# Performance work log

Measured on AMD Instinct MI355X. Metric: run time of the kernel, lower is better.

The kernel has to match this reference:

```python
import jax, jax.numpy as jnp
import numpy as np

D_MODEL = 1024
NUM_HEADS = 16
HEAD_DIM = D_MODEL // NUM_HEADS
N = 4096


def setup_inputs() -> dict:
    key = jax.random.key(0)
    k_x, k_wqkv, k_bqkv, k_wo, k_bo = jax.random.split(key, 5)
    s_in = 1.0 / np.sqrt(D_MODEL)
    return {
        "x": jax.random.normal(k_x, (N, D_MODEL), dtype=jnp.float32),
        "w_qkv": jax.random.uniform(k_wqkv, (D_MODEL, 3 * D_MODEL), jnp.float32, -s_in, s_in),
        "b_qkv": jax.random.uniform(k_bqkv, (3 * D_MODEL,), jnp.float32, -s_in, s_in),
        "w_out": jax.random.uniform(k_wo, (D_MODEL, D_MODEL), jnp.float32, -s_in, s_in),
        "b_out": jax.random.uniform(k_bo, (D_MODEL,), jnp.float32, -s_in, s_in),
    }


def reference(x, w_qkv, b_qkv, w_out, b_out) -> jnp.ndarray:
    n, d = x.shape
    scale = HEAD_DIM ** -0.5
    # fused QKV projection: [N, 3D] -> [3, H, N, hd]
    qkv = (x @ w_qkv + b_qkv).reshape(n, 3, NUM_HEADS, HEAD_DIM).transpose(1, 2, 0, 3)
    q, k, v = qkv[0], qkv[1], qkv[2]
    attn = jax.nn.softmax(jnp.einsum("hnd,hmd->hnm", q, k) * scale, axis=-1)
    out = jnp.einsum("hnm,hmd->hnd", attn, v)  # [H, N, hd]
    out = out.transpose(1, 0, 2).reshape(n, d)
    return out @ w_out + b_out
```

## Files before the change

kernel.cpp:

```cpp
#include <hip/hip_runtime.h>
#include <hip/hip_bf16.h>

using bf16_t = __bf16;
using bf16x4 = __attribute__((ext_vector_type(4))) __bf16;
using bf16x8 = __attribute__((ext_vector_type(8))) __bf16;
using f32x4  = __attribute__((ext_vector_type(4))) float;
using f32x16 = __attribute__((ext_vector_type(16))) float;
using u32x2  = __attribute__((ext_vector_type(2))) unsigned;

#define N_TOK 4096
#define DM    1024
#define NH    16
#define HD    64
#define D3    3072

#if __has_builtin(__builtin_amdgcn_exp2f)
#define EXP2(x) __builtin_amdgcn_exp2f(x)
#else
extern "C" float __ocml_native_exp2_f32(float);
#define EXP2(x) __ocml_native_exp2_f32(x)
#endif

__device__ __forceinline__ void gl_lds16(const void* g, void* l) {
  __builtin_amdgcn_global_load_lds((const __attribute__((address_space(1))) void*)g,
                                   (__attribute__((address_space(3))) void*)l, 16, 0, 0);
}

__device__ __forceinline__ unsigned pkbf(float a, float b) {
  unsigned short la = __builtin_bit_cast(unsigned short, (bf16_t)a);
  unsigned short lb = __builtin_bit_cast(unsigned short, (bf16_t)b);
  return (unsigned)la | ((unsigned)lb << 16);
}

__device__ __forceinline__ bf16x8 mk8(unsigned a, unsigned b, unsigned c, unsigned d) {
  union { unsigned u[4]; bf16x8 v; } t;
  t.u[0] = a; t.u[1] = b; t.u[2] = c; t.u[3] = d;
  return t.v;
}

__device__ __forceinline__ void softmax_blk(const f32x16& sv, bf16x8& apA, bf16x8& apB) {
  float pp[16];
  #pragma unroll
  for (int r = 0; r < 16; r++) pp[r] = EXP2(sv[r]);
  unsigned w00 = pkbf(pp[0], pp[1]),   w01 = pkbf(pp[2], pp[3]);
  unsigned w10 = pkbf(pp[4], pp[5]),   w11 = pkbf(pp[6], pp[7]);
  unsigned w20 = pkbf(pp[8], pp[9]),   w21 = pkbf(pp[10], pp[11]);
  unsigned w30 = pkbf(pp[12], pp[13]), w31 = pkbf(pp[14], pp[15]);
  u32x2 r00 = __builtin_amdgcn_permlane32_swap(w00, w10, false, false);
  u32x2 r01 = __builtin_amdgcn_permlane32_swap(w01, w11, false, false);
  u32x2 r10 = __builtin_amdgcn_permlane32_swap(w20, w30, false, false);
  u32x2 r11 = __builtin_amdgcn_permlane32_swap(w21, w31, false, false);
  apA = mk8(r00[0], r01[0], r00[1], r01[1]);
  apB = mk8(r10[0], r11[0], r10[1], r11[1]);
}

__global__ void k_cvt_x(const float* __restrict__ x, bf16_t* __restrict__ xb) {
  int i = (blockIdx.x * blockDim.x + threadIdx.x) * 8;
  float4 f0 = *(const float4*)(x + i);
  float4 f1 = *(const float4*)(x + i + 4);
  bf16x8 v;
  v[0] = (bf16_t)f0.x; v[1] = (bf16_t)f0.y; v[2] = (bf16_t)f0.z; v[3] = (bf16_t)f0.w;
  v[4] = (bf16_t)f1.x; v[5] = (bf16_t)f1.y; v[6] = (bf16_t)f1.z; v[7] = (bf16_t)f1.w;
  *(bf16x8*)(xb + i) = v;
}

__global__ void k_transpose_cvt(const float* __restrict__ in, bf16_t* __restrict__ outh,
                                int R, int C) {
  __shared__ float tile[64][65];
  int r0 = blockIdx.y * 64, c0 = blockIdx.x * 64;
  int t = threadIdx.x;
  #pragma unroll
  for (int i = 0; i < 16; i++) {
    int idx = i * 256 + t; int r = idx >> 6, c = idx & 63;
    tile[r][c] = in[(size_t)(r0 + r) * C + (c0 + c)];
  }
  __syncthreads();
  #pragma unroll
  for (int i = 0; i < 16; i++) {
    int idx = i * 256 + t; int c = idx >> 6, r = idx & 63;
    outh[(size_t)(c0 + c) * R + (r0 + r)] = (bf16_t)tile[r][c];
  }
}

__global__ __launch_bounds__(256) void k_gemm_qkv(
    const bf16_t* __restrict__ A, const bf16_t* __restrict__ Bt,
    const float* __restrict__ bias, bf16_t* __restrict__ qkv, bf16_t* __restrict__ vT) {
  __shared__ bf16_t As[128 * 32];
  __shared__ bf16_t Bs[128 * 32];
  const int tid = threadIdx.x, wid = tid >> 6, lane = tid & 63;
  const int bid = blockIdx.x;
  const int brow = bid & 31;
  const int bcol = bid >> 5;
  const int wr = wid >> 1, wc = wid & 1;
  const int lrow = lane & 15, lk = (lane >> 4) * 8;

  f32x4 acc[4][4] = {};

  const int c0 = wid * 64 + lane;
  const int c1 = 256 + wid * 64 + lane;
  const bf16_t* Ab = A + (size_t)(brow * 128) * DM;
  const bf16_t* Bb = Bt + (size_t)(bcol * 128) * DM;

  for (int k0 = 0; k0 < DM; k0 += 32) {
    gl_lds16(Ab + (size_t)(c0 >> 2) * DM + k0 + (c0 & 3) * 8, As + (wid * 64) * 8);
    gl_lds16(Ab + (size_t)(c1 >> 2) * DM + k0 + (c1 & 3) * 8, As + (256 + wid * 64) * 8);
    gl_lds16(Bb + (size_t)(c0 >> 2) * DM + k0 + (c0 & 3) * 8, Bs + (wid * 64) * 8);
    gl_lds16(Bb + (size_t)(c1 >> 2) * DM + k0 + (c1 & 3) * 8, Bs + (256 + wid * 64) * 8);
    __syncthreads();
    bf16x8 a[4], b[4];
    #pragma unroll
    for (int m = 0; m < 4; m++) a[m] = *(const bf16x8*)(As + (wr * 64 + m * 16 + lrow) * 32 + lk);
    #pragma unroll
    for (int n = 0; n < 4; n++) b[n] = *(const bf16x8*)(Bs + (wc * 64 + n * 16 + lrow) * 32 + lk);
    #pragma unroll
    for (int m = 0; m < 4; m++)
      #pragma unroll
      for (int n = 0; n < 4; n++)
        acc[m][n] = __builtin_amdgcn_mfma_f32_16x16x32_bf16(a[m], b[n], acc[m][n], 0, 0, 0);
    __syncthreads();
  }

  const int row0 = brow * 128 + wr * 64, col0 = bcol * 128 + wc * 64;
  #pragma unroll
  for (int n = 0; n < 4; n++) {
    int col = col0 + n * 16 + lrow;
    int which = col >> 10, rem = col & 1023;
    int h = rem >> 6, d = rem & 63;
    float bv = bias[col];
    float scl = (which == 0) ? 0.18033688011112042f : 1.0f;
    if (which == 2) {
      bf16_t* ob = vT + ((size_t)h * HD + d) * N_TOK;
      #pragma unroll
      for (int m = 0; m < 4; m++) {
        int tok0 = row0 + m * 16 + (lane >> 4) * 4;
        bf16x4 pk;
        #pragma unroll
        for (int i = 0; i < 4; i++) pk[i] = (bf16_t)(acc[m][n][i] + bv);
        *(bf16x4*)(ob + tok0) = pk;
      }
    } else {
      bf16_t* ob = qkv + (size_t)(which * NH + h) * N_TOK * HD + d;
      #pragma unroll
      for (int m = 0; m < 4; m++)
        #pragma unroll
        for (int i = 0; i < 4; i++) {
          int row = row0 + m * 16 + (lane >> 4) * 4 + i;
          ob[(size_t)row * HD] = (bf16_t)((acc[m][n][i] + bv) * scl);
        }
    }
  }
}

__global__ __launch_bounds__(256, 4) void k_attn(
    const bf16_t* __restrict__ qkv, const bf16_t* __restrict__ vT,
    float* __restrict__ opart, float* __restrict__ lpart, int kv_chunk) {
  __shared__ bf16_t Kss[2][64 * 64];
  __shared__ bf16_t Vts[2][64 * 64];
  const int tid = threadIdx.x, wid = tid >> 6, lane = tid & 63;
  const int qb = blockIdx.x, h = blockIdx.y, kvs = blockIdx.z;
  const bf16_t* Q  = qkv + (size_t)h * N_TOK * HD;
  const bf16_t* K  = qkv + (size_t)(NH + h) * N_TOK * HD;
  const bf16_t* Vt = vT + (size_t)h * HD * N_TOK;
  const int L31 = lane & 31, h5 = lane >> 5, r7 = L31 & 7;

  const int kv_lo = kvs * kv_chunk;
  const int kv_hi = kv_lo + kv_chunk;

  const int sr0 = tid >> 3;
  const int sc0 = (tid & 7) ^ (sr0 & 7);

#define STAGE(B, KV0) do {                                                                  \
    gl_lds16(K  + (size_t)((KV0) + sr0)      * HD + sc0 * 8, &Kss[B][wid * 512]);           \
    gl_lds16(K  + (size_t)((KV0) + 32 + sr0) * HD + sc0 * 8, &Kss[B][2048 + wid * 512]);    \
    gl_lds16(Vt + (size_t)sr0        * N_TOK + (KV0) + sc0 * 8, &Vts[B][wid * 512]);        \
    gl_lds16(Vt + (size_t)(32 + sr0) * N_TOK + (KV0) + sc0 * 8, &Vts[B][2048 + wid * 512]); \
  } while (0)

  bf16x8 aq[4];
  {
    int qrow = qb * 128 + wid * 32 + L31;
    #pragma unroll
    for (int dc = 0; dc < 4; dc++)
      aq[dc] = *(const bf16x8*)(Q + (size_t)qrow * HD + dc * 16 + h5 * 8);
  }
  f32x16 o0 = {}, o1 = {}, l_acc = {};
  f32x16 fz = {};
  asm volatile("" : "+v"(fz));
  bf16x8 ones8;
  #pragma unroll
  for (int j = 0; j < 8; j++) ones8[j] = (bf16_t)1.0f;

  STAGE(0, kv_lo);
  __syncthreads();

  int buf = 0;
  for (int kv0 = kv_lo; kv0 < kv_hi; kv0 += 64) {
    if (kv0 + 64 < kv_hi) STAGE(buf ^ 1, kv0 + 64);
    const bf16_t* kb = &Kss[buf][0] + L31 * 64;
    const bf16_t* vb = &Vts[buf][0] + L31 * 64;

    __builtin_amdgcn_s_setprio(1);
    bf16x8 kf0 = *(const bf16x8*)(kb + (((0 + h5) ^ r7) * 8));
    bf16x8 kf1 = *(const bf16x8*)(kb + 2048 + (((0 + h5) ^ r7) * 8));
    f32x16 s0 = __builtin_amdgcn_mfma_f32_32x32x16_bf16(kf0, aq[0], fz, 0, 0, 0);
    f32x16 s1 = __builtin_amdgcn_mfma_f32_32x32x16_bf16(kf1, aq[0], fz, 0, 0, 0);
    #pragma unroll
    for (int dc = 1; dc < 4; dc++) {
      kf0 = *(const bf16x8*)(kb + (((dc * 2 + h5) ^ r7) * 8));
      s0 = __builtin_amdgcn_mfma_f32_32x32x16_bf16(kf0, aq[dc], s0, 0, 0, 0);
      kf1 = *(const bf16x8*)(kb + 2048 + (((dc * 2 + h5) ^ r7) * 8));
      s1 = __builtin_amdgcn_mfma_f32_32x32x16_bf16(kf1, aq[dc], s1, 0, 0, 0);
    }
    __builtin_amdgcn_s_setprio(0);

    bf16x8 ap0, ap1, ap2, ap3;
    softmax_blk(s0, ap0, ap1);
    __builtin_amdgcn_s_setprio(1);
    {
      bf16x8 vf;
      vf = *(const bf16x8*)(vb + (((0 + h5) ^ r7) * 8));
      o0 = __builtin_amdgcn_mfma_f32_32x32x16_bf16(ap0, vf, o0, 0, 0, 0);
      vf = *(const bf16x8*)(vb + (((2 + h5) ^ r7) * 8));
      o0 = __builtin_amdgcn_mfma_f32_32x32x16_bf16(ap1, vf, o0, 0, 0, 0);
      vf = *(const bf16x8*)(vb + 2048 + (((0 + h5) ^ r7) * 8));
      o1 = __builtin_amdgcn_mfma_f32_32x32x16_bf16(ap0, vf, o1, 0, 0, 0);
      vf = *(const bf16x8*)(vb + 2048 + (((2 + h5) ^ r7) * 8));
      o1 = __builtin_amdgcn_mfma_f32_32x32x16_bf16(ap1, vf, o1, 0, 0, 0);
      l_acc = __builtin_amdgcn_mfma_f32_32x32x16_bf16(ap0, ones8, l_acc, 0, 0, 0);
      l_acc = __builtin_amdgcn_mfma_f32_32x32x16_bf16(ap1, ones8, l_acc, 0, 0, 0);
    }
    __builtin_amdgcn_s_setprio(0);
    softmax_blk(s1, ap2, ap3);
    __builtin_amdgcn_s_setprio(1);
    {
      bf16x8 vf;
      vf = *(const bf16x8*)(vb + (((4 + h5) ^ r7) * 8));
      o0 = __builtin_amdgcn_mfma_f32_32x32x16_bf16(ap2, vf, o0, 0, 0, 0);
      vf = *(const bf16x8*)(vb + (((6 + h5) ^ r7) * 8));
      o0 = __builtin_amdgcn_mfma_f32_32x32x16_bf16(ap3, vf, o0, 0, 0, 0);
      vf = *(const bf16x8*)(vb + 2048 + (((4 + h5) ^ r7) * 8));
      o1 = __builtin_amdgcn_mfma_f32_32x32x16_bf16(ap2, vf, o1, 0, 0, 0);
      vf = *(const bf16x8*)(vb + 2048 + (((6 + h5) ^ r7) * 8));
      o1 = __builtin_amdgcn_mfma_f32_32x32x16_bf16(ap3, vf, o1, 0, 0, 0);
      l_acc = __builtin_amdgcn_mfma_f32_32x32x16_bf16(ap2, ones8, l_acc, 0, 0, 0);
      l_acc = __builtin_amdgcn_mfma_f32_32x32x16_bf16(ap3, ones8, l_acc, 0, 0, 0);
    }
    __builtin_amdgcn_s_setprio(0);

    __syncthreads();
    buf ^= 1;
  }
#undef STAGE

  if (L31 == 0) {
    float* lp = lpart + ((size_t)kvs * NH + h) * N_TOK + qb * 128 + wid * 32;
    #pragma unroll
    for (int r = 0; r < 16; r++)
      lp[(r & 3) + 8 * (r >> 2) + 4 * h5] = l_acc[r];
  }

  float* op = opart + (size_t)kvs * N_TOK * DM;
  #pragma unroll
  for (int r = 0; r < 16; r++) {
    int q32 = (r & 3) + 8 * (r >> 2) + 4 * h5;
    size_t base = (size_t)(qb * 128 + wid * 32 + q32) * DM + h * HD + L31;
    op[base] = o0[r];
    op[base + 32] = o1[r];
  }
}

__global__ __launch_bounds__(256) void k_combine(
    const float* __restrict__ opart, const float* __restrict__ lpart,
    bf16_t* __restrict__ oattn, int nsplit) {
  const int row = blockIdx.x, tid = threadIdx.x;
  const int col = tid * 4;
  const int h = col >> 6;
  const size_t idx = (size_t)row * DM + col;
  float4 a = *(const float4*)(opart + idx);
  float lsum = lpart[(size_t)h * N_TOK + row];
  for (int p = 1; p < nsplit; p++) {
    float4 b = *(const float4*)(opart + (size_t)p * N_TOK * DM + idx);
    a.x += b.x; a.y += b.y; a.z += b.z; a.w += b.w;
    lsum += lpart[((size_t)p * NH + h) * N_TOK + row];
  }
  float rl = 1.0f / lsum;
  bf16x4 hv;
  hv[0] = (bf16_t)(a.x * rl); hv[1] = (bf16_t)(a.y * rl);
  hv[2] = (bf16_t)(a.z * rl); hv[3] = (bf16_t)(a.w * rl);
  *(bf16x4*)(oattn + idx) = hv;
}

__global__ __launch_bounds__(256) void k_gemm_out(
    const bf16_t* __restrict__ A, const bf16_t* __restrict__ Bt,
    const float* __restrict__ bias, float* __restrict__ out) {
  __shared__ bf16_t As[128 * 32];
  __shared__ bf16_t Bs[128 * 32];
  const int tid = threadIdx.x, wid = tid >> 6, lane = tid & 63;
  const int bid = blockIdx.x;
  const int brow = bid & 31;
  const int bcol = bid >> 5;
  const int wr = wid >> 1, wc = wid & 1;
  const int lrow = lane & 15, lk = (lane >> 4) * 8;

  f32x4 acc[4][4] = {};

  const int c0 = wid * 64 + lane;
  const int c1 = 256 + wid * 64 + lane;
  const bf16_t* Ab = A + (size_t)(brow * 128) * DM;
  const bf16_t* Bb = Bt + (size_t)(bcol * 128) * DM;

  for (int k0 = 0; k0 < DM; k0 += 32) {
    gl_lds16(Ab + (size_t)(c0 >> 2) * DM + k0 + (c0 & 3) * 8, As + (wid * 64) * 8);
    gl_lds16(Ab + (size_t)(c1 >> 2) * DM + k0 + (c1 & 3) * 8, As + (256 + wid * 64) * 8);
    gl_lds16(Bb + (size_t)(c0 >> 2) * DM + k0 + (c0 & 3) * 8, Bs + (wid * 64) * 8);
    gl_lds16(Bb + (size_t)(c1 >> 2) * DM + k0 + (c1 & 3) * 8, Bs + (256 + wid * 64) * 8);
    __syncthreads();
    bf16x8 a[4], b[4];
    #pragma unroll
    for (int m = 0; m < 4; m++) a[m] = *(const bf16x8*)(As + (wr * 64 + m * 16 + lrow) * 32 + lk);
    #pragma unroll
    for (int n = 0; n < 4; n++) b[n] = *(const bf16x8*)(Bs + (wc * 64 + n * 16 + lrow) * 32 + lk);
    #pragma unroll
    for (int m = 0; m < 4; m++)
      #pragma unroll
      for (int n = 0; n < 4; n++)
        acc[m][n] = __builtin_amdgcn_mfma_f32_16x16x32_bf16(a[m], b[n], acc[m][n], 0, 0, 0);
    __syncthreads();
  }

  const int row0 = brow * 128 + wr * 64, col0 = bcol * 128 + wc * 64;
  #pragma unroll
  for (int n = 0; n < 4; n++) {
    int col = col0 + n * 16 + lrow;
    float bv = bias[col];
    #pragma unroll
    for (int m = 0; m < 4; m++)
      #pragma unroll
      for (int i = 0; i < 4; i++) {
        int row = row0 + m * 16 + (lane >> 4) * 4 + i;
        out[(size_t)row * DM + col] = acc[m][n][i] + bv;
      }
  }
}

extern "C" void kernel_launch(void* const* d_in, const int* in_sizes, int n_in,
                              void* d_out, int out_size, void* d_ws, size_t ws_size,
                              hipStream_t stream) {
  const float* x     = (const float*)d_in[0];
  const float* w_qkv = (const float*)d_in[1];
  const float* b_qkv = (const float*)d_in[2];
  const float* w_out = (const float*)d_in[3];
  const float* b_out = (const float*)d_in[4];
  float* out = (float*)d_out;

  char* ws = (char*)d_ws;
  bf16_t* qkv     = (bf16_t*)(ws);
  bf16_t* x_bf    = (bf16_t*)(ws + 25165824);
  bf16_t* wqkv_t  = (bf16_t*)(ws + 33554432);
  bf16_t* wout_t  = (bf16_t*)(ws + 39845888);
  bf16_t* attn    = (bf16_t*)(ws + 41943040);
  float*  lpart   = (float*)(ws + 50331648);
  float*  opart   = (float*)(ws + 51380224);
  bf16_t* vT      = qkv + (size_t)2 * NH * N_TOK * HD;

  const size_t OPBASE = 51380224ull;
  const size_t PART = (size_t)N_TOK * DM * 4;
  int nsplit = 1;
  if (ws_size >= OPBASE + 4 * PART) nsplit = 4;
  else if (ws_size >= OPBASE + 2 * PART) nsplit = 2;

  k_cvt_x<<<2048, 256, 0, stream>>>(x, x_bf);
  k_transpose_cvt<<<dim3(48, 16), 256, 0, stream>>>(w_qkv, wqkv_t, DM, D3);
  k_transpose_cvt<<<dim3(16, 16), 256, 0, stream>>>(w_out, wout_t, DM, DM);
  k_gemm_qkv<<<768, 256, 0, stream>>>(x_bf, wqkv_t, b_qkv, qkv, vT);
  k_attn<<<dim3(32, 16, nsplit), 256, 0, stream>>>(qkv, vT, opart, lpart, N_TOK / nsplit);
  k_combine<<<4096, 256, 0, stream>>>(opart, lpart, attn, nsplit);
  k_gemm_out<<<256, 256, 0, stream>>>(attn, wout_t, b_out, out);
}
```

Baseline: 177.6 us.

## Triple-buffer K/V in attention with a single barrier per iteration, cap split at 2

The attention kernel's K/V staging goes from double to triple buffering in LDS. It prefetches two tiles ahead, uses explicit vmcnt waits and one barrier per iteration instead of a trailing __syncthreads, which aims to hide global-load latency and cut synchronisation. Separately, the KV split factor is capped at 2 instead of 4. That halves the combine traffic and the partial writes, but it also halves the attention grid's parallelism. The larger LDS footprint (48KB) may lower occupancy.

```diff
diff --git a/kernel.cpp b/kernel.cpp
--- a/kernel.cpp
+++ b/kernel.cpp
@@ -154,8 +154,9 @@
 __global__ __launch_bounds__(256, 4) void k_attn(
     const bf16_t* __restrict__ qkv, const bf16_t* __restrict__ vT,
     float* __restrict__ opart, float* __restrict__ lpart, int kv_chunk) {
-  __shared__ bf16_t Kss[2][64 * 64];
-  __shared__ bf16_t Vts[2][64 * 64];
+  __shared__ bf16_t smem[3 * 4096 * 2];
+  bf16_t* smK = smem;
+  bf16_t* smV = smem + 12288;
   const int tid = threadIdx.x, wid = tid >> 6, lane = tid & 63;
   const int qb = blockIdx.x, h = blockIdx.y, kvs = blockIdx.z;
   const bf16_t* Q  = qkv + (size_t)h * N_TOK * HD;
@@ -164,16 +165,15 @@
   const int L31 = lane & 31, h5 = lane >> 5, r7 = L31 & 7;
 
   const int kv_lo = kvs * kv_chunk;
-  const int kv_hi = kv_lo + kv_chunk;
 
   const int sr0 = tid >> 3;
   const int sc0 = (tid & 7) ^ (sr0 & 7);
 
-#define STAGE(B, KV0) do {                                                                  \
-    gl_lds16(K  + (size_t)((KV0) + sr0)      * HD + sc0 * 8, &Kss[B][wid * 512]);           \
-    gl_lds16(K  + (size_t)((KV0) + 32 + sr0) * HD + sc0 * 8, &Kss[B][2048 + wid * 512]);    \
-    gl_lds16(Vt + (size_t)sr0        * N_TOK + (KV0) + sc0 * 8, &Vts[B][wid * 512]);        \
-    gl_lds16(Vt + (size_t)(32 + sr0) * N_TOK + (KV0) + sc0 * 8, &Vts[B][2048 + wid * 512]); \
+#define STAGE(ROFF, KV0) do {                                                            \
+    gl_lds16(K  + (size_t)((KV0) + sr0)      * HD + sc0 * 8, smK + (ROFF) + wid * 512);  \
+    gl_lds16(K  + (size_t)((KV0) + 32 + sr0) * HD + sc0 * 8, smK + (ROFF) + 2048 + wid * 512); \
+    gl_lds16(Vt + (size_t)sr0        * N_TOK + (KV0) + sc0 * 8, smV + (ROFF) + wid * 512);     \
+    gl_lds16(Vt + (size_t)(32 + sr0) * N_TOK + (KV0) + sc0 * 8, smV + (ROFF) + 2048 + wid * 512); \
   } while (0)
 
   bf16x8 aq[4];
@@ -191,13 +191,26 @@
   for (int j = 0; j < 8; j++) ones8[j] = (bf16_t)1.0f;
 
   STAGE(0, kv_lo);
-  __syncthreads();
-
-  int buf = 0;
-  for (int kv0 = kv_lo; kv0 < kv_hi; kv0 += 64) {
-    if (kv0 + 64 < kv_hi) STAGE(buf ^ 1, kv0 + 64);
-    const bf16_t* kb = &Kss[buf][0] + L31 * 64;
-    const bf16_t* vb = &Vts[buf][0] + L31 * 64;
+  STAGE(4096, kv_lo + 64);
+
+  const int iters = kv_chunk / 64;
+  int r = 0;
+  int kv_next = kv_lo + 128;
+  for (int i = 0; i < iters; i++) {
+    if (i + 1 < iters) { asm volatile("s_waitcnt vmcnt(4)" ::: "memory"); }
+    else               { asm volatile("s_waitcnt vmcnt(0)" ::: "memory"); }
+    __builtin_amdgcn_sched_barrier(0);
+    __builtin_amdgcn_s_barrier();
+    __builtin_amdgcn_sched_barrier(0);
+
+    if (i + 2 < iters) {
+      int rn = r + 2; if (rn >= 3) rn -= 3;
+      STAGE(rn * 4096, kv_next);
+    }
+    kv_next += 64;
+
+    const bf16_t* kb = smK + r * 4096 + L31 * 64;
+    const bf16_t* vb = smV + r * 4096 + L31 * 64;
 
     __builtin_amdgcn_s_setprio(1);
     bf16x8 kf0 = *(const bf16x8*)(kb + (((0 + h5) ^ r7) * 8));
@@ -247,25 +260,24 @@
     }
     __builtin_amdgcn_s_setprio(0);
 
-    __syncthreads();
-    buf ^= 1;
+    r += 1; if (r == 3) r = 0;
   }
 #undef STAGE
 
   if (L31 == 0) {
     float* lp = lpart + ((size_t)kvs * NH + h) * N_TOK + qb * 128 + wid * 32;
     #pragma unroll
-    for (int r = 0; r < 16; r++)
-      lp[(r & 3) + 8 * (r >> 2) + 4 * h5] = l_acc[r];
+    for (int rr = 0; rr < 16; rr++)
+      lp[(rr & 3) + 8 * (rr >> 2) + 4 * h5] = l_acc[rr];
   }
 
   float* op = opart + (size_t)kvs * N_TOK * DM;
   #pragma unroll
-  for (int r = 0; r < 16; r++) {
-    int q32 = (r & 3) + 8 * (r >> 2) + 4 * h5;
+  for (int rr = 0; rr < 16; rr++) {
+    int q32 = (rr & 3) + 8 * (rr >> 2) + 4 * h5;
     size_t base = (size_t)(qb * 128 + wid * 32 + q32) * DM + h * HD + L31;
-    op[base] = o0[r];
-    op[base + 32] = o1[r];
+    op[base] = o0[rr];
+    op[base + 32] = o1[rr];
   }
 }
 
@@ -365,9 +377,7 @@
 
   const size_t OPBASE = 51380224ull;
   const size_t PART = (size_t)N_TOK * DM * 4;
-  int nsplit = 1;
-  if (ws_size >= OPBASE + 4 * PART) nsplit = 4;
-  else if (ws_size >= OPBASE + 2 * PART) nsplit = 2;
+  const int nsplit = (ws_size >= OPBASE + 2 * PART) ? 2 : 1;
 
   k_cvt_x<<<2048, 256, 0, stream>>>(x, x_bf);
   k_transpose_cvt<<<dim3(48, 16), 256, 0, stream>>>(w_qkv, wqkv_t, DM, D3);
```

Result: no change. 175.0 us (-1.5%).
